# Kernel tuning notes

Measured on AMD Instinct MI355X. Metric: run time of the kernel, lower is better.

## Reference

```python
import jax, jax.numpy as jnp
import numpy as np

NEG = -1e9

def _lstm(x, Wih, Whh, b):
    # x: [B,S,D]; PyTorch gate order i,f,g,o; Wih:[4H,D], Whh:[4H,H], b:[4H]
    B = x.shape[0]
    H = Whh.shape[1]
    def step(carry, xt):
        h, c = carry
        g = xt @ Wih.T + h @ Whh.T + b
        i, f, gg, o = jnp.split(g, 4, axis=-1)
        c = jax.nn.sigmoid(f) * c + jax.nn.sigmoid(i) * jnp.tanh(gg)
        h = jax.nn.sigmoid(o) * jnp.tanh(c)
        return (h, c), h
    init = (jnp.zeros((B, H), x.dtype), jnp.zeros((B, H), x.dtype))
    _, hs = jax.lax.scan(step, init, x.transpose(1, 0, 2))
    return hs.transpose(1, 0, 2)  # [B,S,H]

def _bilstm(x, Wih_f, Whh_f, b_f, Wih_b, Whh_b, b_b):
    fwd = _lstm(x, Wih_f, Whh_f, b_f)
    bwd = jnp.flip(_lstm(jnp.flip(x, 1), Wih_b, Whh_b, b_b), 1)
    return jnp.concatenate([fwd, bwd], axis=-1)

def _windowed_attention(h, attn_W, attn_b, window_size):
    # score(i,j) = W @ [h_i, h_j, h_i*h_j] + b, decomposed exactly:
    #   = h_i@w1 + h_j@w2 + (h_i*w3)@h_j + b, masked to |i-j| <= window
    S = h.shape[1]
    w1, w2, w3 = jnp.split(attn_W[0], 3)
    s1 = h @ w1                                   # [B,S]
    s2 = h @ w2                                   # [B,S]
    cross = jnp.einsum('bid,bjd->bij', h * w3, h)  # [B,S,S]
    scores = s1[:, :, None] + s2[:, None, :] + cross + attn_b[0]
    idx = jnp.arange(S)
    band = jnp.abs(idx[:, None] - idx[None, :]) <= window_size
    scores = jnp.where(band, scores, NEG)
    p = jax.nn.softmax(scores, axis=-1)
    return jnp.einsum('bij,bjd->bid', p, h)       # [B,S,H]

def _forward(x, lstm1_Wih_f, lstm1_Whh_f, lstm1_b_f, lstm1_Wih_b, lstm1_Whh_b, lstm1_b_b,
             fc1_W, fc1_b, attn_W, attn_b,
             lstm2_Wih_f, lstm2_Whh_f, lstm2_b_f, lstm2_Wih_b, lstm2_Whh_b, lstm2_b_b,
             l2_W1, l2_b1, l2_W2, l2_b2, l2_W3, l2_b3, window_size):
    # dropout layers are identity at inference
    lstm_out = _bilstm(x, lstm1_Wih_f, lstm1_Whh_f, lstm1_b_f,
                       lstm1_Wih_b, lstm1_Whh_b, lstm1_b_b)          # [B,S,768]
    h = lstm_out @ fc1_W.T + fc1_b                                    # [B,S,384]
    attn = _windowed_attention(h, attn_W, attn_b, window_size)        # [B,S,384]
    h_cat = jnp.concatenate([h, attn], axis=-1)                       # [B,S,768]
    lstm_out2 = _bilstm(h_cat, lstm2_Wih_f, lstm2_Whh_f, lstm2_b_f,
                        lstm2_Wih_b, lstm2_Whh_b, lstm2_b_b)          # [B,S,768]
    h2 = lstm_out2 @ fc1_W.T + fc1_b                                  # fc1 reused, as in source
    y = jax.nn.relu(h2 @ l2_W1.T + l2_b1)
    y = jax.nn.relu(y @ l2_W2.T + l2_b2)
    return y @ l2_W3.T + l2_b3                                        # [B,S,1]

def setup_inputs() -> dict:
    key = jax.random.key(0)
    ks = iter(jax.random.split(key, 32))
    D, H, B, S = 768, 384, 16, 1024
    sc = 0.02
    def rn(shape):
        return jax.random.normal(next(ks), shape, dtype=jnp.float32) * sc
    inp = {'x': jax.random.normal(next(ks), (B, S, D), dtype=jnp.float32)}
    for name in ('lstm1', 'lstm2'):
        inp[f'{name}_Wih_f'] = rn((4 * H, D)); inp[f'{name}_Whh_f'] = rn((4 * H, H))
        inp[f'{name}_b_f'] = rn((4 * H,))
        inp[f'{name}_Wih_b'] = rn((4 * H, D)); inp[f'{name}_Whh_b'] = rn((4 * H, H))
        inp[f'{name}_b_b'] = rn((4 * H,))
    inp['fc1_W'] = rn((H, D)); inp['fc1_b'] = rn((H,))
    inp['attn_W'] = rn((1, 3 * H)); inp['attn_b'] = rn((1,))
    inp['l2_W1'] = rn((256, H)); inp['l2_b1'] = rn((256,))
    inp['l2_W2'] = rn((96, 256)); inp['l2_b2'] = rn((96,))
    inp['l2_W3'] = rn((1, 96)); inp['l2_b3'] = rn((1,))
    inp['window_size'] = 32
    return inp

def reference(x, lstm1_Wih_f, lstm1_Whh_f, lstm1_b_f, lstm1_Wih_b, lstm1_Whh_b, lstm1_b_b,
              fc1_W, fc1_b, attn_W, attn_b,
              lstm2_Wih_f, lstm2_Whh_f, lstm2_b_f, lstm2_Wih_b, lstm2_Whh_b, lstm2_b_b,
              l2_W1, l2_b1, l2_W2, l2_b2, l2_W3, l2_b3, window_size):
    return _forward(x, lstm1_Wih_f, lstm1_Whh_f, lstm1_b_f, lstm1_Wih_b, lstm1_Whh_b, lstm1_b_b,
                    fc1_W, fc1_b, attn_W, attn_b,
                    lstm2_Wih_f, lstm2_Whh_f, lstm2_b_f, lstm2_Wih_b, lstm2_Whh_b, lstm2_b_b,
                    l2_W1, l2_b1, l2_W2, l2_b2, l2_W3, l2_b3, window_size)
```

## Files before the change

### kernel.cpp

```cpp
#include <hip/hip_runtime.h>
#include <hip/hip_bf16.h>
#include <type_traits>

#define S_LEN 1024
#define BATCH 16
#define HID   384
#define DIN   768

#define GRP 8
#define UPB 48
#define NTHR 384

__device__ __forceinline__ float sigf(float x)     { return 1.f/(1.f + __expf(-x)); }
__device__ __forceinline__ float tanhfast(float x) { return 1.f - 2.f/(__expf(2.f*x) + 1.f); }

__global__ void zero_kernel(unsigned long long* hx)
{
    int i = blockIdx.x * blockDim.x + threadIdx.x;
    if (i < 32*2*HID) hx[i] = 0ull;
}

template<int RELU, typename OT>
__global__ __launch_bounds__(256) void gemm_nt(
    const float* __restrict__ A, int ldA,
    const float* __restrict__ W,
    const float* __restrict__ bias,
    OT* __restrict__ C, int ldC,
    int M, int N, int K)
{
    __shared__ float As[16][132];
    __shared__ float Ws[16][68];
    const int tid = threadIdx.x;
    const int m0 = blockIdx.x * 128;
    const int n0 = blockIdx.y * 64;
    const int tm = (tid & 15) * 8;
    const int tn = (tid >> 4) * 4;

    float acc[8][4];
    #pragma unroll
    for (int i = 0; i < 8; i++)
        #pragma unroll
        for (int j = 0; j < 4; j++) acc[i][j] = 0.f;

    const int lrow = tid >> 2;
    const int lk   = (tid & 3) * 4;

    for (int k0 = 0; k0 < K; k0 += 16) {
        #pragma unroll
        for (int p = 0; p < 2; p++) {
            const int r = lrow + p * 64;
            const float4 av = *(const float4*)(A + (size_t)(m0 + r) * ldA + k0 + lk);
            As[lk+0][r] = av.x; As[lk+1][r] = av.y; As[lk+2][r] = av.z; As[lk+3][r] = av.w;
        }
        {
            float4 wv = make_float4(0.f, 0.f, 0.f, 0.f);
            if (n0 + lrow < N) wv = *(const float4*)(W + (size_t)(n0 + lrow) * K + k0 + lk);
            Ws[lk+0][lrow] = wv.x; Ws[lk+1][lrow] = wv.y; Ws[lk+2][lrow] = wv.z; Ws[lk+3][lrow] = wv.w;
        }
        __syncthreads();
        #pragma unroll
        for (int k = 0; k < 16; k++) {
            const float4 a0 = *(const float4*)&As[k][tm];
            const float4 a1 = *(const float4*)&As[k][tm + 4];
            const float4 bv = *(const float4*)&Ws[k][tn];
            const float am[8] = {a0.x, a0.y, a0.z, a0.w, a1.x, a1.y, a1.z, a1.w};
            const float bb[4] = {bv.x, bv.y, bv.z, bv.w};
            #pragma unroll
            for (int i = 0; i < 8; i++)
                #pragma unroll
                for (int j = 0; j < 4; j++) acc[i][j] += am[i] * bb[j];
        }
        __syncthreads();
    }

    #pragma unroll
    for (int i = 0; i < 8; i++) {
        const int m = m0 + tm + i;
        #pragma unroll
        for (int j = 0; j < 4; j++) {
            const int n = n0 + tn + j;
            if (n < N) {
                float v = acc[i][j] + bias[n];
                if (RELU) v = fmaxf(v, 0.f);
                if constexpr (std::is_same_v<OT, __hip_bfloat16>)
                    C[(size_t)m * ldC + n] = __float2bfloat16(v);
                else
                    C[(size_t)m * ldC + n] = v;
            }
        }
    }
}

__global__ __launch_bounds__(NTHR) void lstm_scan(
    const __hip_bfloat16* __restrict__ gatesF, const __hip_bfloat16* __restrict__ gatesB,
    const float* __restrict__ WhhF,            const float* __restrict__ WhhB,
    float* __restrict__ out, unsigned long long* hx_all, int epoch)
{
    __shared__ float hl[2][HID];

    const int blk = blockIdx.x;
    const int g   = blk & 31;
    const int m   = blk >> 5;
    const int dir = g >> 4;
    const int b   = g & 15;
    const int u0  = m * UPB;

    const __hip_bfloat16* gates = dir ? gatesB : gatesF;
    const float* Whh = dir ? WhhB : WhhF;
    unsigned long long* hx = hx_all + g * (2 * HID);

    const int tid = threadIdx.x;
    const int rr  = tid >> 3;
    const int ss  = tid & 7;
    const int ug  = u0 + rr;
    const bool owner = (ss == 0);

    float w[4][UPB];
    #pragma unroll
    for (int gt = 0; gt < 4; gt++) {
        const float* wp = Whh + ((size_t)gt * HID + ug) * HID + ss * 4;
        #pragma unroll
        for (int j = 0; j < 12; j++) {
            const float4 v = *(const float4*)(wp + 32 * j);
            w[gt][4*j+0] = v.x; w[gt][4*j+1] = v.y;
            w[gt][4*j+2] = v.z; w[gt][4*j+3] = v.w;
        }
    }

    float c_state = 0.f;
    const unsigned tbase = (unsigned)epoch * 2048u;

    for (int t = 0; t < S_LEN; t++) {
        const int tt = dir ? (S_LEN - 1 - t) : t;

        float gx0 = 0.f, gx1 = 0.f, gx2 = 0.f, gx3 = 0.f;
        if (owner) {
            const __hip_bfloat16* gp = gates + ((size_t)(b * S_LEN + tt)) * (4 * HID) + ug;
            gx0 = __bfloat162float(gp[0]);
            gx1 = __bfloat162float(gp[HID]);
            gx2 = __bfloat162float(gp[2 * HID]);
            gx3 = __bfloat162float(gp[3 * HID]);
        }

        if (t == 0) {
            if (tid < 128) {
                hl[0][tid] = 0.f; hl[0][tid + 128] = 0.f; hl[0][tid + 256] = 0.f;
            }
        } else if (tid < 128) {
            const unsigned long long* src = hx + ((t + 1) & 1) * HID;
            float* dst = hl[t & 1];
            const unsigned tgt = tbase + (unsigned)t;
            int pend = 7;
            long guard = 0;
            do {
                if (pend & 1) {
                    const unsigned long long q = __hip_atomic_load(src + tid,
                        __ATOMIC_RELAXED, __HIP_MEMORY_SCOPE_AGENT);
                    if ((unsigned)(q >> 32) >= tgt) {
                        dst[tid] = __uint_as_float((unsigned)q); pend &= ~1;
                    }
                }
                if (pend & 2) {
                    const unsigned long long q = __hip_atomic_load(src + tid + 128,
                        __ATOMIC_RELAXED, __HIP_MEMORY_SCOPE_AGENT);
                    if ((unsigned)(q >> 32) >= tgt) {
                        dst[tid + 128] = __uint_as_float((unsigned)q); pend &= ~2;
                    }
                }
                if (pend & 4) {
                    const unsigned long long q = __hip_atomic_load(src + tid + 256,
                        __ATOMIC_RELAXED, __HIP_MEMORY_SCOPE_AGENT);
                    if ((unsigned)(q >> 32) >= tgt) {
                        dst[tid + 256] = __uint_as_float((unsigned)q); pend &= ~4;
                    }
                }
                if (!pend) break;
                __builtin_amdgcn_s_sleep(1);
            } while (++guard < (1L << 22));
        }
        __syncthreads();

        const float* hsl = hl[t & 1];
        float a0 = 0.f, a1 = 0.f, a2 = 0.f, a3 = 0.f;
        #pragma unroll
        for (int j = 0; j < 12; j++) {
            const float4 h4 = *(const float4*)(hsl + ss * 4 + 32 * j);
            const float hh[4] = {h4.x, h4.y, h4.z, h4.w};
            #pragma unroll
            for (int e = 0; e < 4; e++) {
                a0 += w[0][4*j+e] * hh[e];
                a1 += w[1][4*j+e] * hh[e];
                a2 += w[2][4*j+e] * hh[e];
                a3 += w[3][4*j+e] * hh[e];
            }
        }
        a0 += __shfl_xor(a0, 1, 64); a0 += __shfl_xor(a0, 2, 64); a0 += __shfl_xor(a0, 4, 64);
        a1 += __shfl_xor(a1, 1, 64); a1 += __shfl_xor(a1, 2, 64); a1 += __shfl_xor(a1, 4, 64);
        a2 += __shfl_xor(a2, 1, 64); a2 += __shfl_xor(a2, 2, 64); a2 += __shfl_xor(a2, 4, 64);
        a3 += __shfl_xor(a3, 1, 64); a3 += __shfl_xor(a3, 2, 64); a3 += __shfl_xor(a3, 4, 64);

        if (owner) {
            const float ii = sigf(a0 + gx0);
            const float ff = sigf(a1 + gx1);
            const float gg = tanhfast(a2 + gx2);
            const float oo = sigf(a3 + gx3);
            c_state = ff * c_state + ii * gg;
            const float hn = oo * tanhfast(c_state);
            const unsigned long long pk =
                ((unsigned long long)(tbase + (unsigned)t + 1u) << 32) |
                (unsigned long long)__float_as_uint(hn);
            __hip_atomic_store(hx + (t & 1) * HID + ug, pk,
                               __ATOMIC_RELAXED, __HIP_MEMORY_SCOPE_AGENT);
            out[((size_t)(b * S_LEN + tt)) * (2 * HID) + dir * HID + ug] = hn;
        }
    }
}

__global__ __launch_bounds__(256) void attn_win(
    const float* __restrict__ hcat,
    const float* __restrict__ attnW,
    float* __restrict__ ocat,
    const int* __restrict__ wsz_p)
{
    __shared__ float q[HID];
    __shared__ float sc[96];
    __shared__ float p[96];
    const int blk = blockIdx.x;
    const int b = blk >> 10, i = blk & 1023;
    const int W = *wsz_p;
    const int jlo = max(i - W, 0), jhi = min(i + W, S_LEN - 1);
    const int nj = jhi - jlo + 1;
    const int tid = threadIdx.x;
    const float* hrow = hcat + (size_t)b * S_LEN * 768;

    if (tid < 96) {
        const float4 hv = *(const float4*)(hrow + (size_t)i * 768 + tid * 4);
        const float4 w3 = *(const float4*)(attnW + 768 + tid * 4);
        const float4 w2 = *(const float4*)(attnW + 384 + tid * 4);
        float4 r;
        r.x = hv.x*w3.x + w2.x; r.y = hv.y*w3.y + w2.y;
        r.z = hv.z*w3.z + w2.z; r.w = hv.w*w3.w + w2.w;
        *(float4*)(q + tid * 4) = r;
    }
    __syncthreads();

    const int wv = tid >> 6, lane = tid & 63;
    for (int jj = wv; jj < nj; jj += 4) {
        const float* hj = hrow + (size_t)(jlo + jj) * 768;
        float s = 0.f;
        #pragma unroll
        for (int c = 0; c < 6; c++) { const int d = lane + 64*c; s += q[d] * hj[d]; }
        #pragma unroll
        for (int st = 1; st < 64; st <<= 1) s += __shfl_xor(s, st, 64);
        if (lane == 0) sc[jj] = s;
    }
    __syncthreads();

    if (tid < 64) {
        float v1 = (tid < nj) ? sc[tid] : -3e38f;
        float v2 = (64 + tid < nj) ? sc[64 + tid] : -3e38f;
        float m = fmaxf(v1, v2);
        #pragma unroll
        for (int st = 1; st < 64; st <<= 1) m = fmaxf(m, __shfl_xor(m, st, 64));
        float e1 = (tid < nj) ? __expf(v1 - m) : 0.f;
        float e2 = (64 + tid < nj) ? __expf(v2 - m) : 0.f;
        float sum = e1 + e2;
        #pragma unroll
        for (int st = 1; st < 64; st <<= 1) sum += __shfl_xor(sum, st, 64);
        const float inv = 1.f / sum;
        if (tid < nj) p[tid] = e1 * inv;
        if (64 + tid < nj) p[64 + tid] = e2 * inv;
    }
    __syncthreads();

    if (tid < 192) {
        const int d = tid * 2;
        float s0 = 0.f, s1 = 0.f;
        for (int jj = 0; jj < nj; jj++) {
            const float* hj = hrow + (size_t)(jlo + jj) * 768 + d;
            const float pj = p[jj];
            s0 += pj * hj[0]; s1 += pj * hj[1];
        }
        float* o = ocat + (size_t)b * S_LEN * 768 + (size_t)i * 768 + 384 + d;
        o[0] = s0; o[1] = s1;
    }
}

__global__ __launch_bounds__(256) void final_dot(
    const float* __restrict__ y2, const float* __restrict__ W3,
    const float* __restrict__ b3, float* __restrict__ outp)
{
    __shared__ float w[96];
    const int tid = threadIdx.x;
    if (tid < 96) w[tid] = W3[tid];
    __syncthreads();
    const int r = blockIdx.x * 256 + tid;
    const float* row = y2 + (size_t)r * 96;
    float s = 0.f;
    #pragma unroll
    for (int c = 0; c < 24; c++) {
        const float4 v = ((const float4*)row)[c];
        s += v.x*w[c*4] + v.y*w[c*4+1] + v.z*w[c*4+2] + v.w*w[c*4+3];
    }
    outp[r] = s + b3[0];
}

extern "C" void kernel_launch(void* const* d_in, const int* in_sizes, int n_in,
                              void* d_out, int out_size, void* d_ws, size_t ws_size,
                              hipStream_t stream)
{
    const float* x        = (const float*)d_in[0];
    const float* l1_Wih_f = (const float*)d_in[1];
    const float* l1_Whh_f = (const float*)d_in[2];
    const float* l1_b_f   = (const float*)d_in[3];
    const float* l1_Wih_b = (const float*)d_in[4];
    const float* l1_Whh_b = (const float*)d_in[5];
    const float* l1_b_b   = (const float*)d_in[6];
    const float* l2_Wih_f = (const float*)d_in[7];
    const float* l2_Whh_f = (const float*)d_in[8];
    const float* l2_b_f   = (const float*)d_in[9];
    const float* l2_Wih_b = (const float*)d_in[10];
    const float* l2_Whh_b = (const float*)d_in[11];
    const float* l2_b_b   = (const float*)d_in[12];
    const float* fc1_W    = (const float*)d_in[13];
    const float* fc1_b    = (const float*)d_in[14];
    const float* attn_W   = (const float*)d_in[15];
    const float* w1       = (const float*)d_in[17];
    const float* b1       = (const float*)d_in[18];
    const float* w2       = (const float*)d_in[19];
    const float* b2       = (const float*)d_in[20];
    const float* w3       = (const float*)d_in[21];
    const float* b3       = (const float*)d_in[22];
    const int*   wsz      = (const int*)d_in[23];

    char* wsb = (char*)d_ws;
    __hip_bfloat16*     gF  = (__hip_bfloat16*)(wsb);
    __hip_bfloat16*     gB  = (__hip_bfloat16*)(wsb +  50331648);
    float*              seq = (float*)(wsb + 100663296);
    float*              hct = (float*)(wsb + 150994944);
    unsigned long long* hx  = (unsigned long long*)(wsb + 201326592);
    float*              h2  = (float*)(wsb);
    float*              y1  = (float*)(wsb +  50331648);
    float*              y2  = (float*)(wsb +  50331648 + 16777216);

    const int M = BATCH * S_LEN;
    dim3 tb(256);

    zero_kernel<<<dim3(96), tb, 0, stream>>>(hx);
    gemm_nt<0, __hip_bfloat16><<<dim3(M/128, 24), tb, 0, stream>>>(x, DIN, l1_Wih_f, l1_b_f, gF, 1536, M, 1536, DIN);
    gemm_nt<0, __hip_bfloat16><<<dim3(M/128, 24), tb, 0, stream>>>(x, DIN, l1_Wih_b, l1_b_b, gB, 1536, M, 1536, DIN);
    lstm_scan<<<dim3(256), dim3(NTHR), 0, stream>>>(gF, gB, l1_Whh_f, l1_Whh_b, seq, hx, 0);

    gemm_nt<0, float><<<dim3(M/128, 6), tb, 0, stream>>>(seq, 768, fc1_W, fc1_b, hct, 768, M, 384, 768);
    attn_win<<<dim3(M), tb, 0, stream>>>(hct, attn_W, hct, wsz);

    gemm_nt<0, __hip_bfloat16><<<dim3(M/128, 24), tb, 0, stream>>>(hct, 768, l2_Wih_f, l2_b_f, gF, 1536, M, 1536, 768);
    gemm_nt<0, __hip_bfloat16><<<dim3(M/128, 24), tb, 0, stream>>>(hct, 768, l2_Wih_b, l2_b_b, gB, 1536, M, 1536, 768);
    lstm_scan<<<dim3(256), dim3(NTHR), 0, stream>>>(gF, gB, l2_Whh_f, l2_Whh_b, seq, hx, 1);

    gemm_nt<0, float><<<dim3(M/128, 6), tb, 0, stream>>>(seq, 768, fc1_W, fc1_b, h2, 384, M, 384, 768);
    gemm_nt<1, float><<<dim3(M/128, 4), tb, 0, stream>>>(h2, 384, w1, b1, y1, 256, M, 256, 384);
    gemm_nt<1, float><<<dim3(M/128, 2), tb, 0, stream>>>(y1, 256, w2, b2, y2, 96, M, 96, 256);
    final_dot<<<dim3(M/256), tb, 0, stream>>>(y2, w3, b3, (float*)d_out);
}
```

Before: 7.310 ms.

## Move LSTM recurrent weights from registers into fp16 LDS image

The scan kernel's 192 fp32 recurrent weights per thread no longer live in registers. They are converted to fp16 and stored in a 144KB dynamic shared-memory image laid out per thread, and each step reads them back from LDS and converts them to float before the dot product. This removes the heavy register pressure and likely spilling of the register-resident weights, at the cost of LDS reads every timestep and reduced weight precision. It relies on a large dynamic LDS allocation per block (about 147KB plus the h buffers), which the hardware must support.

```diff
diff --git a/kernel.cpp b/kernel.cpp
--- a/kernel.cpp
+++ b/kernel.cpp
@@ -1,5 +1,6 @@
 #include <hip/hip_runtime.h>
 #include <hip/hip_bf16.h>
+#include <hip/hip_fp16.h>
 #include <type_traits>
 
 #define S_LEN 1024
@@ -96,7 +97,9 @@
     const float* __restrict__ WhhF,            const float* __restrict__ WhhB,
     float* __restrict__ out, unsigned long long* hx_all, int epoch)
 {
-    __shared__ float hl[2][HID];
+    extern __shared__ char smem_raw[];
+    __half* wimg = (__half*)smem_raw;
+    float*  hl   = (float*)(smem_raw + 147456);
 
     const int blk = blockIdx.x;
     const int g   = blk & 31;
@@ -115,15 +118,18 @@
     const int ug  = u0 + rr;
     const bool owner = (ss == 0);
 
-    float w[4][UPB];
     #pragma unroll
     for (int gt = 0; gt < 4; gt++) {
-        const float* wp = Whh + ((size_t)gt * HID + ug) * HID + ss * 4;
-        #pragma unroll
-        for (int j = 0; j < 12; j++) {
-            const float4 v = *(const float4*)(wp + 32 * j);
-            w[gt][4*j+0] = v.x; w[gt][4*j+1] = v.y;
-            w[gt][4*j+2] = v.z; w[gt][4*j+3] = v.w;
+        const float* wp = Whh + ((size_t)(gt * HID + ug)) * HID + ss * 8;
+        #pragma unroll
+        for (int jj = 0; jj < 6; jj++) {
+            const float4 va = *(const float4*)(wp + 64 * jj);
+            const float4 vb = *(const float4*)(wp + 64 * jj + 4);
+            __half2* dst = (__half2*)&wimg[(size_t)(((gt * 6) + jj) * NTHR + tid) * 8];
+            dst[0] = __halves2half2(__float2half(va.x), __float2half(va.y));
+            dst[1] = __halves2half2(__float2half(va.z), __float2half(va.w));
+            dst[2] = __halves2half2(__float2half(vb.x), __float2half(vb.y));
+            dst[3] = __halves2half2(__float2half(vb.z), __float2half(vb.w));
         }
     }
 
@@ -144,11 +150,11 @@
 
         if (t == 0) {
             if (tid < 128) {
-                hl[0][tid] = 0.f; hl[0][tid + 128] = 0.f; hl[0][tid + 256] = 0.f;
+                hl[tid] = 0.f; hl[tid + 128] = 0.f; hl[tid + 256] = 0.f;
             }
         } else if (tid < 128) {
             const unsigned long long* src = hx + ((t + 1) & 1) * HID;
-            float* dst = hl[t & 1];
+            float* dst = hl + (t & 1) * HID;
             const unsigned tgt = tbase + (unsigned)t;
             int pend = 7;
             long guard = 0;
@@ -180,18 +186,25 @@
         }
         __syncthreads();
 
-        const float* hsl = hl[t & 1];
+        const float* hsl = hl + (t & 1) * HID;
         float a0 = 0.f, a1 = 0.f, a2 = 0.f, a3 = 0.f;
         #pragma unroll
-        for (int j = 0; j < 12; j++) {
-            const float4 h4 = *(const float4*)(hsl + ss * 4 + 32 * j);
-            const float hh[4] = {h4.x, h4.y, h4.z, h4.w};
+        for (int jj = 0; jj < 6; jj++) {
+            const float4 h40 = *(const float4*)(hsl + ss * 8 + 64 * jj);
+            const float4 h41 = *(const float4*)(hsl + ss * 8 + 64 * jj + 4);
+            const float hh[8] = {h40.x, h40.y, h40.z, h40.w, h41.x, h41.y, h41.z, h41.w};
             #pragma unroll
-            for (int e = 0; e < 4; e++) {
-                a0 += w[0][4*j+e] * hh[e];
-                a1 += w[1][4*j+e] * hh[e];
-                a2 += w[2][4*j+e] * hh[e];
-                a3 += w[3][4*j+e] * hh[e];
+            for (int gt = 0; gt < 4; gt++) {
+                const __half2* wv2 = (const __half2*)&wimg[(size_t)(((gt * 6) + jj) * NTHR + tid) * 8];
+                const __half2 w0 = wv2[0], w1 = wv2[1], w2 = wv2[2], w3 = wv2[3];
+                float s = __low2float(w0) * hh[0] + __high2float(w0) * hh[1]
+                        + __low2float(w1) * hh[2] + __high2float(w1) * hh[3]
+                        + __low2float(w2) * hh[4] + __high2float(w2) * hh[5]
+                        + __low2float(w3) * hh[6] + __high2float(w3) * hh[7];
+                if (gt == 0) a0 += s;
+                else if (gt == 1) a1 += s;
+                else if (gt == 2) a2 += s;
+                else a3 += s;
             }
         }
         a0 += __shfl_xor(a0, 1, 64); a0 += __shfl_xor(a0, 2, 64); a0 += __shfl_xor(a0, 4, 64);
@@ -344,19 +357,20 @@
     float*              y2  = (float*)(wsb +  50331648 + 16777216);
 
     const int M = BATCH * S_LEN;
+    const int scan_lds = 147456 + 2 * HID * 4;
     dim3 tb(256);
 
     zero_kernel<<<dim3(96), tb, 0, stream>>>(hx);
     gemm_nt<0, __hip_bfloat16><<<dim3(M/128, 24), tb, 0, stream>>>(x, DIN, l1_Wih_f, l1_b_f, gF, 1536, M, 1536, DIN);
     gemm_nt<0, __hip_bfloat16><<<dim3(M/128, 24), tb, 0, stream>>>(x, DIN, l1_Wih_b, l1_b_b, gB, 1536, M, 1536, DIN);
-    lstm_scan<<<dim3(256), dim3(NTHR), 0, stream>>>(gF, gB, l1_Whh_f, l1_Whh_b, seq, hx, 0);
+    lstm_scan<<<dim3(256), dim3(NTHR), scan_lds, stream>>>(gF, gB, l1_Whh_f, l1_Whh_b, seq, hx, 0);
 
     gemm_nt<0, float><<<dim3(M/128, 6), tb, 0, stream>>>(seq, 768, fc1_W, fc1_b, hct, 768, M, 384, 768);
     attn_win<<<dim3(M), tb, 0, stream>>>(hct, attn_W, hct, wsz);
 
     gemm_nt<0, __hip_bfloat16><<<dim3(M/128, 24), tb, 0, stream>>>(hct, 768, l2_Wih_f, l2_b_f, gF, 1536, M, 1536, 768);
     gemm_nt<0, __hip_bfloat16><<<dim3(M/128, 24), tb, 0, stream>>>(hct, 768, l2_Wih_b, l2_b_b, gB, 1536, M, 1536, 768);
-    lstm_scan<<<dim3(256), dim3(NTHR), 0, stream>>>(gF, gB, l2_Whh_f, l2_Whh_b, seq, hx, 1);
+    lstm_scan<<<dim3(256), dim3(NTHR), scan_lds, stream>>>(gF, gB, l2_Whh_f, l2_Whh_b, seq, hx, 1);
 
     gemm_nt<0, float><<<dim3(M/128, 6), tb, 0, stream>>>(seq, 768, fc1_W, fc1_b, h2, 384, M, 384, 768);
     gemm_nt<1, float><<<dim3(M/128, 4), tb, 0, stream>>>(h2, 384, w1, b1, y1, 256, M, 256, 384);
```

Result: slower. 11.27 ms (+54.2%).

## Use fp16 MFMA for LSTM input GEMMs and stream fp16 recurrent weights

Applied to the files above, without the earlier changes.

Adds an MFMA-based fp16 GEMM with swizzled LDS tiles for the four large input-projection GEMMs, replacing the scalar fp32 tiled GEMM. The LSTM scan kernel no longer keeps the recurrent weights in registers. It instead reads fp16-converted weights (produced by a new prep kernel into the hct scratch buffer) from global memory every timestep. This is meant to cut GEMM time and register pressure. In exchange it adds per-step memory traffic on the latency-critical scan and reduces precision to fp16.

```diff
diff --git a/kernel.cpp b/kernel.cpp
--- a/kernel.cpp
+++ b/kernel.cpp
@@ -1,5 +1,6 @@
 #include <hip/hip_runtime.h>
 #include <hip/hip_bf16.h>
+#include <hip/hip_fp16.h>
 #include <type_traits>
 
 #define S_LEN 1024
@@ -14,10 +15,116 @@
 __device__ __forceinline__ float sigf(float x)     { return 1.f/(1.f + __expf(-x)); }
 __device__ __forceinline__ float tanhfast(float x) { return 1.f - 2.f/(__expf(2.f*x) + 1.f); }
 
+__device__ __forceinline__ __half2 unpackh2(float f) {
+    return __builtin_bit_cast(__half2, f);
+}
+
+typedef __attribute__((ext_vector_type(8))) _Float16 f16x8;
+typedef __attribute__((ext_vector_type(4))) float f32x4;
+
 __global__ void zero_kernel(unsigned long long* hx)
 {
     int i = blockIdx.x * blockDim.x + threadIdx.x;
     if (i < 32*2*HID) hx[i] = 0ull;
+}
+
+__global__ void prep16(const float* __restrict__ wf, const float* __restrict__ wb,
+                       __half* __restrict__ o)
+{
+    int i = blockIdx.x * 256 + threadIdx.x;
+    if (i < 147456) {
+        const float4 a = ((const float4*)wf)[i];
+        const float4 b = ((const float4*)wb)[i];
+        __half2* of = (__half2*)o;
+        of[2*i]   = __halves2half2(__float2half(a.x), __float2half(a.y));
+        of[2*i+1] = __halves2half2(__float2half(a.z), __float2half(a.w));
+        __half2* ob = (__half2*)(o + 589824);
+        ob[2*i]   = __halves2half2(__float2half(b.x), __float2half(b.y));
+        ob[2*i+1] = __halves2half2(__float2half(b.z), __float2half(b.w));
+    }
+}
+
+__global__ __launch_bounds__(256) void gemm_f16(
+    const float* __restrict__ A, int ldA,
+    const float* __restrict__ W,
+    const float* __restrict__ bias,
+    __hip_bfloat16* __restrict__ C, int ldC,
+    int K)
+{
+    __shared__ char Al[128 * 128];
+    __shared__ char Bl[128 * 128];
+    const int tid  = threadIdx.x;
+    const int m0   = blockIdx.x * 128;
+    const int n0   = blockIdx.y * 128;
+    const int wid  = tid >> 6, lane = tid & 63;
+    const int wm   = (wid >> 1) * 64, wn = (wid & 1) * 64;
+    const int fr   = lane & 15, fq = lane >> 4;
+
+    f32x4 acc[4][4] = {};
+
+    const int srow = tid >> 1;
+    const int sseg = (tid & 1) * 32;
+
+    for (int k0 = 0; k0 < K; k0 += 64) {
+        {
+            const float* ap = A + (size_t)(m0 + srow) * ldA + k0 + sseg;
+            const float* wp = W + (size_t)(n0 + srow) * K   + k0 + sseg;
+            _Float16 ta[32], tw[32];
+            #pragma unroll
+            for (int q = 0; q < 8; q++) {
+                const float4 va = *(const float4*)(ap + q * 4);
+                const float4 vw = *(const float4*)(wp + q * 4);
+                ta[4*q+0] = (_Float16)va.x; ta[4*q+1] = (_Float16)va.y;
+                ta[4*q+2] = (_Float16)va.z; ta[4*q+3] = (_Float16)va.w;
+                tw[4*q+0] = (_Float16)vw.x; tw[4*q+1] = (_Float16)vw.y;
+                tw[4*q+2] = (_Float16)vw.z; tw[4*q+3] = (_Float16)vw.w;
+            }
+            const int xr = (srow & 7) << 4;
+            #pragma unroll
+            for (int c = 0; c < 4; c++) {
+                const int col = (sseg * 2 + c * 16) ^ xr;
+                *(f16x8*)(Al + srow * 128 + col) = *(f16x8*)&ta[c * 8];
+                *(f16x8*)(Bl + srow * 128 + col) = *(f16x8*)&tw[c * 8];
+            }
+        }
+        __syncthreads();
+
+        #pragma unroll
+        for (int kc = 0; kc < 2; kc++) {
+            f16x8 af[4], bf[4];
+            #pragma unroll
+            for (int mt = 0; mt < 4; mt++) {
+                const int r = wm + mt * 16 + fr;
+                af[mt] = *(const f16x8*)(Al + r * 128 + ((kc * 64 + fq * 16) ^ ((r & 7) << 4)));
+            }
+            #pragma unroll
+            for (int nt = 0; nt < 4; nt++) {
+                const int r = wn + nt * 16 + fr;
+                bf[nt] = *(const f16x8*)(Bl + r * 128 + ((kc * 64 + fq * 16) ^ ((r & 7) << 4)));
+            }
+            #pragma unroll
+            for (int mt = 0; mt < 4; mt++)
+                #pragma unroll
+                for (int nt = 0; nt < 4; nt++)
+                    acc[mt][nt] = __builtin_amdgcn_mfma_f32_16x16x32_f16(
+                        af[mt], bf[nt], acc[mt][nt], 0, 0, 0);
+        }
+        __syncthreads();
+    }
+
+    #pragma unroll
+    for (int mt = 0; mt < 4; mt++) {
+        #pragma unroll
+        for (int nt = 0; nt < 4; nt++) {
+            const int n = n0 + wn + nt * 16 + fr;
+            const float bv = bias[n];
+            #pragma unroll
+            for (int j = 0; j < 4; j++) {
+                const int m = m0 + wm + mt * 16 + fq * 4 + j;
+                C[(size_t)m * ldC + n] = __float2bfloat16(acc[mt][nt][j] + bv);
+            }
+        }
+    }
 }
 
 template<int RELU, typename OT>
@@ -93,7 +200,7 @@
 
 __global__ __launch_bounds__(NTHR) void lstm_scan(
     const __hip_bfloat16* __restrict__ gatesF, const __hip_bfloat16* __restrict__ gatesB,
-    const float* __restrict__ WhhF,            const float* __restrict__ WhhB,
+    const __half* __restrict__ wh16,
     float* __restrict__ out, unsigned long long* hx_all, int epoch)
 {
     __shared__ float hl[2][HID];
@@ -106,7 +213,7 @@
     const int u0  = m * UPB;
 
     const __hip_bfloat16* gates = dir ? gatesB : gatesF;
-    const float* Whh = dir ? WhhB : WhhF;
+    const __half* wh = wh16 + (size_t)dir * 589824;
     unsigned long long* hx = hx_all + g * (2 * HID);
 
     const int tid = threadIdx.x;
@@ -114,18 +221,6 @@
     const int ss  = tid & 7;
     const int ug  = u0 + rr;
     const bool owner = (ss == 0);
-
-    float w[4][UPB];
-    #pragma unroll
-    for (int gt = 0; gt < 4; gt++) {
-        const float* wp = Whh + ((size_t)gt * HID + ug) * HID + ss * 4;
-        #pragma unroll
-        for (int j = 0; j < 12; j++) {
-            const float4 v = *(const float4*)(wp + 32 * j);
-            w[gt][4*j+0] = v.x; w[gt][4*j+1] = v.y;
-            w[gt][4*j+2] = v.z; w[gt][4*j+3] = v.w;
-        }
-    }
 
     float c_state = 0.f;
     const unsigned tbase = (unsigned)epoch * 2048u;
@@ -183,15 +278,22 @@
         const float* hsl = hl[t & 1];
         float a0 = 0.f, a1 = 0.f, a2 = 0.f, a3 = 0.f;
         #pragma unroll
-        for (int j = 0; j < 12; j++) {
-            const float4 h4 = *(const float4*)(hsl + ss * 4 + 32 * j);
-            const float hh[4] = {h4.x, h4.y, h4.z, h4.w};
-            #pragma unroll
-            for (int e = 0; e < 4; e++) {
-                a0 += w[0][4*j+e] * hh[e];
-                a1 += w[1][4*j+e] * hh[e];
-                a2 += w[2][4*j+e] * hh[e];
-                a3 += w[3][4*j+e] * hh[e];
+        for (int jj = 0; jj < 6; jj++) {
+            const float4 h40 = *(const float4*)(hsl + ss * 8 + 64 * jj);
+            const float4 h41 = *(const float4*)(hsl + ss * 8 + 64 * jj + 4);
+            #pragma unroll
+            for (int gt = 0; gt < 4; gt++) {
+                const float4 wv = *(const float4*)(wh + ((size_t)(gt * HID + ug)) * HID + ss * 8 + 64 * jj);
+                const __half2 p0 = unpackh2(wv.x), p1 = unpackh2(wv.y),
+                              p2 = unpackh2(wv.z), p3 = unpackh2(wv.w);
+                float s = __low2float(p0) * h40.x + __high2float(p0) * h40.y
+                        + __low2float(p1) * h40.z + __high2float(p1) * h40.w
+                        + __low2float(p2) * h41.x + __high2float(p2) * h41.y
+                        + __low2float(p3) * h41.z + __high2float(p3) * h41.w;
+                if (gt == 0) a0 += s;
+                else if (gt == 1) a1 += s;
+                else if (gt == 2) a2 += s;
+                else a3 += s;
             }
         }
         a0 += __shfl_xor(a0, 1, 64); a0 += __shfl_xor(a0, 2, 64); a0 += __shfl_xor(a0, 4, 64);
@@ -342,21 +444,24 @@
     float*              h2  = (float*)(wsb);
     float*              y1  = (float*)(wsb +  50331648);
     float*              y2  = (float*)(wsb +  50331648 + 16777216);
+    __half*             w16 = (__half*)hct;
 
     const int M = BATCH * S_LEN;
     dim3 tb(256);
 
     zero_kernel<<<dim3(96), tb, 0, stream>>>(hx);
-    gemm_nt<0, __hip_bfloat16><<<dim3(M/128, 24), tb, 0, stream>>>(x, DIN, l1_Wih_f, l1_b_f, gF, 1536, M, 1536, DIN);
-    gemm_nt<0, __hip_bfloat16><<<dim3(M/128, 24), tb, 0, stream>>>(x, DIN, l1_Wih_b, l1_b_b, gB, 1536, M, 1536, DIN);
-    lstm_scan<<<dim3(256), dim3(NTHR), 0, stream>>>(gF, gB, l1_Whh_f, l1_Whh_b, seq, hx, 0);
+    prep16<<<dim3(576), tb, 0, stream>>>(l1_Whh_f, l1_Whh_b, w16);
+    gemm_f16<<<dim3(M/128, 12), tb, 0, stream>>>(x, DIN, l1_Wih_f, l1_b_f, gF, 1536, DIN);
+    gemm_f16<<<dim3(M/128, 12), tb, 0, stream>>>(x, DIN, l1_Wih_b, l1_b_b, gB, 1536, DIN);
+    lstm_scan<<<dim3(256), dim3(NTHR), 0, stream>>>(gF, gB, w16, seq, hx, 0);
 
     gemm_nt<0, float><<<dim3(M/128, 6), tb, 0, stream>>>(seq, 768, fc1_W, fc1_b, hct, 768, M, 384, 768);
     attn_win<<<dim3(M), tb, 0, stream>>>(hct, attn_W, hct, wsz);
 
-    gemm_nt<0, __hip_bfloat16><<<dim3(M/128, 24), tb, 0, stream>>>(hct, 768, l2_Wih_f, l2_b_f, gF, 1536, M, 1536, 768);
-    gemm_nt<0, __hip_bfloat16><<<dim3(M/128, 24), tb, 0, stream>>>(hct, 768, l2_Wih_b, l2_b_b, gB, 1536, M, 1536, 768);
-    lstm_scan<<<dim3(256), dim3(NTHR), 0, stream>>>(gF, gB, l2_Whh_f, l2_Whh_b, seq, hx, 1);
+    gemm_f16<<<dim3(M/128, 12), tb, 0, stream>>>(hct, 768, l2_Wih_f, l2_b_f, gF, 1536, 768);
+    gemm_f16<<<dim3(M/128, 12), tb, 0, stream>>>(hct, 768, l2_Wih_b, l2_b_b, gB, 1536, 768);
+    prep16<<<dim3(576), tb, 0, stream>>>(l2_Whh_f, l2_Whh_b, w16);
+    lstm_scan<<<dim3(256), dim3(NTHR), 0, stream>>>(gF, gB, w16, seq, hx, 1);
 
     gemm_nt<0, float><<<dim3(M/128, 6), tb, 0, stream>>>(seq, 768, fc1_W, fc1_b, h2, 384, M, 384, 768);
     gemm_nt<1, float><<<dim3(M/128, 4), tb, 0, stream>>>(h2, 384, w1, b1, y1, 256, M, 256, 384);
```

Result: faster. 6.198 ms (-15.2%).
